# Kernel tuning notes

Measured on AMD Instinct MI355X. Metric: run time of the kernel, lower is better.

## Reference

```python
import jax, jax.numpy as jnp
import numpy as np

NB_OBJECTS = 3
DIM_BODY = 10
DIM_OBJECT = 15
DIM_OBJ_FEAT = NB_OBJECTS + DIM_OBJECT  # 18
DIM_PHI_IN = 54
HID = 256
DIM_PHI_OUT = 256
DIM_RHO_OUT = 1
B = 65536

# (o1, o2) object pair and (j, k) predicate indices, as in the torch code
PAIRS = [((0, 1), (3, 5)), ((0, 2), (4, 7)), ((1, 2), (6, 8))]


def setup_inputs() -> dict:
    key = jax.random.key(0)
    ks = jax.random.split(key, 24)
    inp = {
        "obs": jax.random.normal(ks[0], (B, 55), dtype=jnp.float32),
        "ag": jax.random.uniform(ks[1], (B, 9), dtype=jnp.float32),
        "g": jax.random.uniform(ks[2], (B, 9), dtype=jnp.float32),
        "anchor_g": jax.random.uniform(ks[3], (B, 9), dtype=jnp.float32),
        "act": jax.random.normal(ks[4], (B, 4), dtype=jnp.float32),
    }
    s = 0.05
    # PhiCriticDeepSet: two independent 2-layer MLPs (streams 1 and 2)
    inp["w1"] = jax.random.normal(ks[5], (DIM_PHI_IN, HID), dtype=jnp.float32) * s
    inp["b1"] = jnp.zeros((HID,), dtype=jnp.float32)
    inp["w2"] = jax.random.normal(ks[6], (HID, DIM_PHI_OUT), dtype=jnp.float32) * s
    inp["b2"] = jnp.zeros((DIM_PHI_OUT,), dtype=jnp.float32)
    inp["w3"] = jax.random.normal(ks[7], (DIM_PHI_IN, HID), dtype=jnp.float32) * s
    inp["b3"] = jnp.zeros((HID,), dtype=jnp.float32)
    inp["w4"] = jax.random.normal(ks[8], (HID, DIM_PHI_OUT), dtype=jnp.float32) * s
    inp["b4"] = jnp.zeros((DIM_PHI_OUT,), dtype=jnp.float32)
    # RhoCriticDeepSet: two independent 2-layer heads
    inp["w5"] = jax.random.normal(ks[9], (DIM_PHI_OUT, HID), dtype=jnp.float32) * s
    inp["b5"] = jnp.zeros((HID,), dtype=jnp.float32)
    inp["w6"] = jax.random.normal(ks[10], (HID, DIM_RHO_OUT), dtype=jnp.float32) * s
    inp["b6"] = jnp.zeros((DIM_RHO_OUT,), dtype=jnp.float32)
    inp["w7"] = jax.random.normal(ks[11], (DIM_PHI_OUT, HID), dtype=jnp.float32) * s
    inp["b7"] = jnp.zeros((HID,), dtype=jnp.float32)
    inp["w8"] = jax.random.normal(ks[12], (HID, DIM_RHO_OUT), dtype=jnp.float32) * s
    inp["b8"] = jnp.zeros((DIM_RHO_OUT,), dtype=jnp.float32)
    return inp


def _build_pair_inputs(obs, ag, g, act, anchor_g):
    """combinations_trick branch: data-dependent gather of goal bits and object pairs."""
    bs = obs.shape[0]
    obs_body = obs[:, :DIM_BODY]
    eye = jnp.eye(NB_OBJECTS, dtype=obs.dtype)
    # obs_objects: [3, B, 18] = one-hot(3) ++ object state(15)
    obs_objects = jnp.stack([
        jnp.concatenate([jnp.broadcast_to(eye[i], (bs, NB_OBJECTS)),
                         obs[:, DIM_BODY + DIM_OBJECT * i: DIM_BODY + DIM_OBJECT * (i + 1)]],
                        axis=1)
        for i in range(NB_OBJECTS)], axis=0)
    bidx = jnp.arange(bs)
    inputs = []
    for i, ((o1, o2), (j, k)) in enumerate(PAIRS):
        # selector = anchor_g @ [e_j, e_k] difference = anchor_g[:, j] - anchor_g[:, k]
        sel = (anchor_g[:, j] - anchor_g[:, k]) >= 0  # [B] bool
        # idxs_bits[i] = [i, j] where sel else [i, k]
        bit2 = jnp.where(sel, j, k)  # [B] int
        ag_pair = jnp.stack([ag[:, i], ag[bidx, bit2]], axis=1)  # [B, 2]
        g_pair = jnp.stack([g[:, i], g[bidx, bit2]], axis=1)     # [B, 2]
        # idxs_objects[i] = [o1, o2] where sel else [o2, o1]
        oi = jnp.where(sel, o1, o2)  # [B]
        oj = jnp.where(sel, o2, o1)
        obj_first = obs_objects[oi, bidx]   # [B, 18] gather along object axis
        obj_second = obs_objects[oj, bidx]  # [B, 18]
        inputs.append(jnp.concatenate(
            [ag_pair, g_pair, obs_body, obj_first, obj_second, act], axis=1))
    return jnp.stack(inputs)  # [3, B, 54]


def reference(obs, ag, g, anchor_g, act,
              w1, b1, w2, b2, w3, b3, w4, b4,
              w5, b5, w6, b6, w7, b7, w8, b8):
    inp = _build_pair_inputs(obs, ag, g, act, anchor_g)  # [3, B, 54]
    # PhiCriticDeepSet (two relu-relu streams)
    x1 = jax.nn.relu(jnp.einsum('pbi,ih->pbh', jax.nn.relu(jnp.einsum('pbd,dh->pbh', inp, w1) + b1), w2) + b2)
    x2 = jax.nn.relu(jnp.einsum('pbi,ih->pbh', jax.nn.relu(jnp.einsum('pbd,dh->pbh', inp, w3) + b3), w4) + b4)
    s1 = x1.sum(axis=0)  # [B, 256] deepset sum over pairs
    s2 = x2.sum(axis=0)
    # RhoCriticDeepSet readouts
    q1 = jax.nn.relu(s1 @ w5 + b5) @ w6 + b6  # [B, 1]
    q2 = jax.nn.relu(s2 @ w7 + b7) @ w8 + b8  # [B, 1]
    return (q1, q2)
```

## Files before the change

### kernel.cpp

```cpp
#include <hip/hip_runtime.h>

typedef unsigned short u16;
typedef unsigned int   u32;

using bf8 = __attribute__((ext_vector_type(8))) __bf16;
using f4  = __attribute__((ext_vector_type(4))) float;

__device__ __forceinline__ float b2f(u16 u) {
    union { u32 i; float f; } v; v.i = ((u32)u) << 16; return v.f;
}
__device__ __forceinline__ u16 f2b(float f) {
    union { float f; u32 i; } v; v.f = f;
    u32 x = v.i;
    x += 0x7fffu + ((x >> 16) & 1u);
    return (u16)(x >> 16);
}

__global__ void swz_all(const float* __restrict__ w1, const float* __restrict__ w3,
                        const float* __restrict__ w2, const float* __restrict__ w4,
                        const float* __restrict__ w5, const float* __restrict__ w7,
                        u16* __restrict__ ws) {
    int bid = blockIdx.x;
    const float* src; u16* dst; int kmax; int rel;
    if      (bid <  32) { src = w1; dst = ws;          kmax = 54;  rel = bid;       }
    else if (bid <  64) { src = w3; dst = ws + 16384;  kmax = 54;  rel = bid - 32;  }
    else if (bid < 192) { src = w2; dst = ws + 32768;  kmax = 256; rel = bid - 64;  }
    else if (bid < 320) { src = w4; dst = ws + 98304;  kmax = 256; rel = bid - 192; }
    else if (bid < 448) { src = w5; dst = ws + 163840; kmax = 256; rel = bid - 320; }
    else                { src = w7; dst = ws + 229376; kmax = 256; rel = bid - 448; }
    int kt = rel >> 4, ct = rel & 15, lane = threadIdx.x;
    int n = ct * 16 + (lane & 15);
    int kbase = kt * 32 + (lane >> 4) * 8;
    u16* d = dst + (size_t)(rel * 64 + lane) * 8;
    #pragma unroll
    for (int j = 0; j < 8; ++j) {
        int k = kbase + j;
        d[j] = (k < kmax) ? f2b(src[k * 256 + n]) : (u16)0;
    }
}

__global__ __launch_bounds__(256, 2) void critic_kernel(
    const float* __restrict__ obs, const float* __restrict__ ag,
    const float* __restrict__ g,   const float* __restrict__ anchor,
    const float* __restrict__ act,
    const float* __restrict__ b1,  const float* __restrict__ b2,
    const float* __restrict__ b3,  const float* __restrict__ b4,
    const float* __restrict__ b5,  const float* __restrict__ b7,
    const float* __restrict__ w6,  const float* __restrict__ b6,
    const float* __restrict__ w8,  const float* __restrict__ b8,
    const u16* __restrict__ wsz, float* __restrict__ out, int B) {

    __shared__ u16 inp_lds[96 * 72];
    __shared__ u16 h_lds[96 * 264];

    const int t    = threadIdx.x;
    const int lane = t & 63;
    const int wave = t >> 6;
    const int lr   = lane & 15;
    const int lg   = lane >> 4;
    const int wg   = blockIdx.x;

    if (t < 96) {
        const int O1[3] = {0, 0, 1}, O2[3] = {1, 2, 2};
        const int JA[3] = {3, 4, 6}, KA[3] = {5, 7, 8};
        int p = t / 32, bl = t % 32;
        int b = wg * 32 + bl;
        int j = JA[p], k = KA[p];
        bool sel = (anchor[b * 9 + j] - anchor[b * 9 + k]) >= 0.0f;
        int bit2 = sel ? j : k;
        int oi = sel ? O1[p] : O2[p];
        int oj = sel ? O2[p] : O1[p];
        u16* row = &inp_lds[t * 72];
        row[0] = f2b(ag[b * 9 + p]);
        row[1] = f2b(ag[b * 9 + bit2]);
        row[2] = f2b(g[b * 9 + p]);
        row[3] = f2b(g[b * 9 + bit2]);
        for (int c = 0; c < 10; ++c) row[4 + c] = f2b(obs[b * 55 + c]);
        const u16 ONE = 0x3F80;
        row[14] = (oi == 0) ? ONE : 0; row[15] = (oi == 1) ? ONE : 0; row[16] = (oi == 2) ? ONE : 0;
        for (int c = 0; c < 15; ++c) row[17 + c] = f2b(obs[b * 55 + 10 + 15 * oi + c]);
        row[32] = (oj == 0) ? ONE : 0; row[33] = (oj == 1) ? ONE : 0; row[34] = (oj == 2) ? ONE : 0;
        for (int c = 0; c < 15; ++c) row[35 + c] = f2b(obs[b * 55 + 10 + 15 * oj + c]);
        for (int c = 0; c < 4; ++c)  row[50 + c] = f2b(act[b * 4 + c]);
        for (int c = 54; c < 72; ++c) row[c] = 0;
    }
    __syncthreads();

    f4  sacc[2][4];
    u32 s1p[2][4][2];

    for (int net = 0; net < 2; ++net) {
        const u16* Wl1 = wsz + (net ? 16384 : 0);
        const u16* Wl2 = wsz + 32768 + (net ? 65536 : 0);
        const float* bl1 = net ? b3 : b1;
        const float* bl2 = net ? b4 : b2;

        f4 acc[6][4];
        #pragma unroll
        for (int rt = 0; rt < 6; ++rt)
            #pragma unroll
            for (int c = 0; c < 4; ++c) acc[rt][c] = (f4){0.f, 0.f, 0.f, 0.f};
        #pragma unroll
        for (int kt = 0; kt < 2; ++kt) {
            bf8 bfr[4];
            #pragma unroll
            for (int c = 0; c < 4; ++c)
                bfr[c] = *(const bf8*)(Wl1 + (size_t)(((kt * 16 + wave * 4 + c) * 64 + lane) * 8));
            #pragma unroll
            for (int rt = 0; rt < 6; ++rt) {
                bf8 afr = *(const bf8*)(&inp_lds[(rt * 16 + lr) * 72 + kt * 32 + lg * 8]);
                #pragma unroll
                for (int c = 0; c < 4; ++c)
                    acc[rt][c] = __builtin_amdgcn_mfma_f32_16x16x32_bf16(afr, bfr[c], acc[rt][c], 0, 0, 0);
            }
        }
        #pragma unroll
        for (int c = 0; c < 4; ++c) {
            float bias = bl1[(wave * 4 + c) * 16 + lr];
            #pragma unroll
            for (int rt = 0; rt < 6; ++rt)
                #pragma unroll
                for (int r = 0; r < 4; ++r) {
                    float x = acc[rt][c][r] + bias;
                    h_lds[(rt * 16 + lg * 4 + r) * 264 + (wave * 4 + c) * 16 + lr] = f2b(fmaxf(x, 0.f));
                }
        }
        __syncthreads();

        f4 acc2[6][4];
        #pragma unroll
        for (int rt = 0; rt < 6; ++rt)
            #pragma unroll
            for (int c = 0; c < 4; ++c) acc2[rt][c] = (f4){0.f, 0.f, 0.f, 0.f};
        #pragma unroll
        for (int ks = 0; ks < 8; ++ks) {
            bf8 bfr[4];
            #pragma unroll
            for (int c = 0; c < 4; ++c)
                bfr[c] = *(const bf8*)(Wl2 + (size_t)(((ks * 16 + wave * 4 + c) * 64 + lane) * 8));
            #pragma unroll
            for (int rt = 0; rt < 6; ++rt) {
                bf8 afr = *(const bf8*)(&h_lds[(rt * 16 + lr) * 264 + ks * 32 + lg * 8]);
                #pragma unroll
                for (int c = 0; c < 4; ++c)
                    acc2[rt][c] = __builtin_amdgcn_mfma_f32_16x16x32_bf16(afr, bfr[c], acc2[rt][c], 0, 0, 0);
            }
        }
        #pragma unroll
        for (int c = 0; c < 4; ++c) {
            float bias = bl2[(wave * 4 + c) * 16 + lr];
            #pragma unroll
            for (int s = 0; s < 2; ++s) {
                f4 sv = (f4){0.f, 0.f, 0.f, 0.f};
                #pragma unroll
                for (int p = 0; p < 3; ++p)
                    #pragma unroll
                    for (int r = 0; r < 4; ++r)
                        sv[r] += fmaxf(acc2[p * 2 + s][c][r] + bias, 0.f);
                if (net == 0) {
                    s1p[s][c][0] = (u32)f2b(sv[0]) | ((u32)f2b(sv[1]) << 16);
                    s1p[s][c][1] = (u32)f2b(sv[2]) | ((u32)f2b(sv[3]) << 16);
                } else {
                    sacc[s][c] = sv;
                }
            }
        }
        __syncthreads();
    }

    #pragma unroll
    for (int s = 0; s < 2; ++s)
        #pragma unroll
        for (int c = 0; c < 4; ++c) {
            int col = (wave * 4 + c) * 16 + lr;
            #pragma unroll
            for (int r = 0; r < 4; ++r) {
                int rowo = (s * 16 + lg * 4 + r) * 264 + col;
                h_lds[rowo]        = (u16)(s1p[s][c][r >> 1] >> ((r & 1) * 16));
                h_lds[8448 + rowo] = f2b(sacc[s][c][r]);
            }
        }
    __syncthreads();

    for (int net = 0; net < 2; ++net) {
        const u16* Wr = wsz + 163840 + net * 65536;
        const float* br = net ? b7 : b5;
        const int soff = net ? 8448 : 0;
        const int hoff = net ? 0 : 16896;
        f4 racc[2][4];
        #pragma unroll
        for (int rt = 0; rt < 2; ++rt)
            #pragma unroll
            for (int c = 0; c < 4; ++c) racc[rt][c] = (f4){0.f, 0.f, 0.f, 0.f};
        #pragma unroll
        for (int ks = 0; ks < 8; ++ks) {
            bf8 bfr[4];
            #pragma unroll
            for (int c = 0; c < 4; ++c)
                bfr[c] = *(const bf8*)(Wr + (size_t)(((ks * 16 + wave * 4 + c) * 64 + lane) * 8));
            #pragma unroll
            for (int rt = 0; rt < 2; ++rt) {
                bf8 afr = *(const bf8*)(&h_lds[soff + (rt * 16 + lr) * 264 + ks * 32 + lg * 8]);
                #pragma unroll
                for (int c = 0; c < 4; ++c)
                    racc[rt][c] = __builtin_amdgcn_mfma_f32_16x16x32_bf16(afr, bfr[c], racc[rt][c], 0, 0, 0);
            }
        }
        #pragma unroll
        for (int c = 0; c < 4; ++c) {
            float bias = br[(wave * 4 + c) * 16 + lr];
            #pragma unroll
            for (int rt = 0; rt < 2; ++rt)
                #pragma unroll
                for (int r = 0; r < 4; ++r) {
                    float x = fmaxf(racc[rt][c][r] + bias, 0.f);
                    h_lds[hoff + (rt * 16 + lg * 4 + r) * 264 + (wave * 4 + c) * 16 + lr] = f2b(x);
                }
        }
        __syncthreads();
    }

    if (t < 64) {
        int net = t >> 5, r = t & 31;
        const float* wv = net ? w8 : w6;
        const int hoff = net ? 0 : 16896;
        float q = net ? b8[0] : b6[0];
        #pragma unroll 8
        for (int kk = 0; kk < 256; ++kk)
            q += b2f(h_lds[hoff + r * 264 + kk]) * wv[kk];
        out[net * B + wg * 32 + r] = q;
    }
}

extern "C" void kernel_launch(void* const* d_in, const int* in_sizes, int n_in,
                              void* d_out, int out_size, void* d_ws, size_t ws_size,
                              hipStream_t stream) {
    const float* obs = (const float*)d_in[0];
    const float* ag  = (const float*)d_in[1];
    const float* g   = (const float*)d_in[2];
    const float* anc = (const float*)d_in[3];
    const float* act = (const float*)d_in[4];
    const float* w1  = (const float*)d_in[5];
    const float* b1  = (const float*)d_in[6];
    const float* w2  = (const float*)d_in[7];
    const float* b2  = (const float*)d_in[8];
    const float* w3  = (const float*)d_in[9];
    const float* b3  = (const float*)d_in[10];
    const float* w4  = (const float*)d_in[11];
    const float* b4  = (const float*)d_in[12];
    const float* w5  = (const float*)d_in[13];
    const float* b5  = (const float*)d_in[14];
    const float* w6  = (const float*)d_in[15];
    const float* b6  = (const float*)d_in[16];
    const float* w7  = (const float*)d_in[17];
    const float* b7  = (const float*)d_in[18];
    const float* w8  = (const float*)d_in[19];
    const float* b8  = (const float*)d_in[20];
    u16* ws   = (u16*)d_ws;
    float* out = (float*)d_out;
    int B = in_sizes[0] / 55;

    swz_all<<<576, 64, 0, stream>>>(w1, w3, w2, w4, w5, w7, ws);
    critic_kernel<<<(B + 31) / 32, 256, 0, stream>>>(obs, ag, g, anc, act,
                                                     b1, b2, b3, b4, b5, b7,
                                                     w6, b6, w8, b8, ws, out, B);
}
```

Before: 219.1 us.

## Coalesce input staging, fuse rho heads, parallelize final dot, retile weight swizzle

Inputs for each 32-row block are now loaded with coalesced strided loops into a shared staging area, and pair rows are built from LDS instead of scattered global reads. The two rho readout GEMMs are merged into one loop so both weight sets are loaded together, which removes a barrier pass. The final 256-wide dot products are split across all four waves and reduced through LDS rather than computed serially by 64 threads. The weight swizzle kernel now uses float4 coalesced loads through a shared slab with fewer, larger blocks. The cost is more shared-memory traffic and extra barriers at the start of the kernel.

```diff
diff --git a/kernel.cpp b/kernel.cpp
--- a/kernel.cpp
+++ b/kernel.cpp
@@ -1,4 +1,5 @@
 #include <hip/hip_runtime.h>
+#include <hip/hip_bf16.h>
 
 typedef unsigned short u16;
 typedef unsigned int   u32;
@@ -15,29 +16,59 @@
     x += 0x7fffu + ((x >> 16) & 1u);
     return (u16)(x >> 16);
 }
+__device__ __forceinline__ u32 pk2(float lo, float hi) {
+    union { __hip_bfloat162 h; u32 u; } v;
+    v.h = __float22bfloat162_rn(make_float2(lo, hi));
+    return v.u;
+}
 
 __global__ void swz_all(const float* __restrict__ w1, const float* __restrict__ w3,
                         const float* __restrict__ w2, const float* __restrict__ w4,
                         const float* __restrict__ w5, const float* __restrict__ w7,
                         u16* __restrict__ ws) {
-    int bid = blockIdx.x;
-    const float* src; u16* dst; int kmax; int rel;
-    if      (bid <  32) { src = w1; dst = ws;          kmax = 54;  rel = bid;       }
-    else if (bid <  64) { src = w3; dst = ws + 16384;  kmax = 54;  rel = bid - 32;  }
-    else if (bid < 192) { src = w2; dst = ws + 32768;  kmax = 256; rel = bid - 64;  }
-    else if (bid < 320) { src = w4; dst = ws + 98304;  kmax = 256; rel = bid - 192; }
-    else if (bid < 448) { src = w5; dst = ws + 163840; kmax = 256; rel = bid - 320; }
-    else                { src = w7; dst = ws + 229376; kmax = 256; rel = bid - 448; }
-    int kt = rel >> 4, ct = rel & 15, lane = threadIdx.x;
-    int n = ct * 16 + (lane & 15);
-    int kbase = kt * 32 + (lane >> 4) * 8;
-    u16* d = dst + (size_t)(rel * 64 + lane) * 8;
+    __shared__ u16 slab[32 * 270];
+    int b = blockIdx.x, t = threadIdx.x;
+    const float* src; u16* dst; int kmax, kt;
+    if      (b <  2) { src = w1; dst = ws;          kmax = 54;  kt = b;      }
+    else if (b <  4) { src = w3; dst = ws + 16384;  kmax = 54;  kt = b - 2;  }
+    else if (b < 12) { src = w2; dst = ws + 32768;  kmax = 256; kt = b - 4;  }
+    else if (b < 20) { src = w4; dst = ws + 98304;  kmax = 256; kt = b - 12; }
+    else if (b < 28) { src = w5; dst = ws + 163840; kmax = 256; kt = b - 20; }
+    else             { src = w7; dst = ws + 229376; kmax = 256; kt = b - 28; }
+
     #pragma unroll
-    for (int j = 0; j < 8; ++j) {
-        int k = kbase + j;
-        d[j] = (k < kmax) ? f2b(src[k * 256 + n]) : (u16)0;
-    }
-}
+    for (int it = 0; it < 8; ++it) {
+        int flat = it * 1024 + t * 4;
+        int row = flat >> 8, col = flat & 255;
+        int k = kt * 32 + row;
+        float4 v = make_float4(0.f, 0.f, 0.f, 0.f);
+        if (k < kmax) v = *(const float4*)(src + k * 256 + col);
+        u32* sp = (u32*)&slab[row * 270 + col];
+        sp[0] = pk2(v.x, v.y);
+        sp[1] = pk2(v.z, v.w);
+    }
+    __syncthreads();
+
+    int lane = t & 63, wave = t >> 6, lr = lane & 15, kg = lane >> 4;
+    #pragma unroll
+    for (int i = 0; i < 4; ++i) {
+        int ct = wave * 4 + i;
+        u16 v[8];
+        #pragma unroll
+        for (int j = 0; j < 8; ++j)
+            v[j] = slab[(kg * 8 + j) * 270 + ct * 16 + lr];
+        uint4 o;
+        o.x = (u32)v[0] | ((u32)v[1] << 16);
+        o.y = (u32)v[2] | ((u32)v[3] << 16);
+        o.z = (u32)v[4] | ((u32)v[5] << 16);
+        o.w = (u32)v[6] | ((u32)v[7] << 16);
+        *(uint4*)(dst + (size_t)(((kt * 16 + ct) * 64 + lane) * 8)) = o;
+    }
+}
+
+#define H_OFF 6912
+#define RH0   (H_OFF + 16896)
+#define RH1   (H_OFF + 16)
 
 __global__ __launch_bounds__(256, 2) void critic_kernel(
     const float* __restrict__ obs, const float* __restrict__ ag,
@@ -50,8 +81,7 @@
     const float* __restrict__ w8,  const float* __restrict__ b8,
     const u16* __restrict__ wsz, float* __restrict__ out, int B) {
 
-    __shared__ u16 inp_lds[96 * 72];
-    __shared__ u16 h_lds[96 * 264];
+    __shared__ u16 pool[32256];
 
     const int t    = threadIdx.x;
     const int lane = t & 63;
@@ -60,29 +90,51 @@
     const int lg   = lane >> 4;
     const int wg   = blockIdx.x;
 
+    const int STG = H_OFF;
+    for (int i = t; i < 1760; i += 256) {
+        int b = i / 55, c = i - b * 55;
+        pool[STG + b * 56 + c] = f2b(obs[wg * 1760 + i]);
+    }
+    for (int i = t; i < 288; i += 256) {
+        int b = i / 9, c = i - b * 9;
+        pool[STG + 1792 + b * 10 + c] = f2b(ag[wg * 288 + i]);
+    }
+    for (int i = t; i < 288; i += 256) {
+        int b = i / 9, c = i - b * 9;
+        pool[STG + 2112 + b * 10 + c] = f2b(g[wg * 288 + i]);
+    }
+    if (t < 128)
+        pool[STG + 2432 + t] = f2b(act[wg * 128 + t]);
+    for (int i = t; i < 288; i += 256) {
+        int b = i / 9, c = i - b * 9;
+        ((u32*)pool)[(STG + 2560) / 2 + b * 10 + c] = __float_as_uint(anchor[wg * 288 + i]);
+    }
+    __syncthreads();
+
     if (t < 96) {
         const int O1[3] = {0, 0, 1}, O2[3] = {1, 2, 2};
         const int JA[3] = {3, 4, 6}, KA[3] = {5, 7, 8};
         int p = t / 32, bl = t % 32;
-        int b = wg * 32 + bl;
         int j = JA[p], k = KA[p];
-        bool sel = (anchor[b * 9 + j] - anchor[b * 9 + k]) >= 0.0f;
+        float aj = __uint_as_float(((u32*)pool)[(STG + 2560) / 2 + bl * 10 + j]);
+        float ak = __uint_as_float(((u32*)pool)[(STG + 2560) / 2 + bl * 10 + k]);
+        bool sel = (aj - ak) >= 0.0f;
         int bit2 = sel ? j : k;
         int oi = sel ? O1[p] : O2[p];
         int oj = sel ? O2[p] : O1[p];
-        u16* row = &inp_lds[t * 72];
-        row[0] = f2b(ag[b * 9 + p]);
-        row[1] = f2b(ag[b * 9 + bit2]);
-        row[2] = f2b(g[b * 9 + p]);
-        row[3] = f2b(g[b * 9 + bit2]);
-        for (int c = 0; c < 10; ++c) row[4 + c] = f2b(obs[b * 55 + c]);
+        u16* row = &pool[t * 72];
+        row[0] = pool[STG + 1792 + bl * 10 + p];
+        row[1] = pool[STG + 1792 + bl * 10 + bit2];
+        row[2] = pool[STG + 2112 + bl * 10 + p];
+        row[3] = pool[STG + 2112 + bl * 10 + bit2];
+        for (int c = 0; c < 10; ++c) row[4 + c] = pool[STG + bl * 56 + c];
         const u16 ONE = 0x3F80;
         row[14] = (oi == 0) ? ONE : 0; row[15] = (oi == 1) ? ONE : 0; row[16] = (oi == 2) ? ONE : 0;
-        for (int c = 0; c < 15; ++c) row[17 + c] = f2b(obs[b * 55 + 10 + 15 * oi + c]);
+        for (int c = 0; c < 15; ++c) row[17 + c] = pool[STG + bl * 56 + 10 + 15 * oi + c];
         row[32] = (oj == 0) ? ONE : 0; row[33] = (oj == 1) ? ONE : 0; row[34] = (oj == 2) ? ONE : 0;
-        for (int c = 0; c < 15; ++c) row[35 + c] = f2b(obs[b * 55 + 10 + 15 * oj + c]);
-        for (int c = 0; c < 4; ++c)  row[50 + c] = f2b(act[b * 4 + c]);
-        for (int c = 54; c < 72; ++c) row[c] = 0;
+        for (int c = 0; c < 15; ++c) row[35 + c] = pool[STG + bl * 56 + 10 + 15 * oj + c];
+        for (int c = 0; c < 4; ++c)  row[50 + c] = pool[STG + 2432 + bl * 4 + c];
+        for (int c = 54; c < 64; ++c) row[c] = 0;
     }
     __syncthreads();
 
@@ -108,7 +160,7 @@
                 bfr[c] = *(const bf8*)(Wl1 + (size_t)(((kt * 16 + wave * 4 + c) * 64 + lane) * 8));
             #pragma unroll
             for (int rt = 0; rt < 6; ++rt) {
-                bf8 afr = *(const bf8*)(&inp_lds[(rt * 16 + lr) * 72 + kt * 32 + lg * 8]);
+                bf8 afr = *(const bf8*)(&pool[(rt * 16 + lr) * 72 + kt * 32 + lg * 8]);
                 #pragma unroll
                 for (int c = 0; c < 4; ++c)
                     acc[rt][c] = __builtin_amdgcn_mfma_f32_16x16x32_bf16(afr, bfr[c], acc[rt][c], 0, 0, 0);
@@ -118,12 +170,15 @@
         for (int c = 0; c < 4; ++c) {
             float bias = bl1[(wave * 4 + c) * 16 + lr];
             #pragma unroll
-            for (int rt = 0; rt < 6; ++rt)
-                #pragma unroll
-                for (int r = 0; r < 4; ++r) {
-                    float x = acc[rt][c][r] + bias;
-                    h_lds[(rt * 16 + lg * 4 + r) * 264 + (wave * 4 + c) * 16 + lr] = f2b(fmaxf(x, 0.f));
-                }
+            for (int rt = 0; rt < 6; ++rt) {
+                u32 p01 = pk2(fmaxf(acc[rt][c][0] + bias, 0.f), fmaxf(acc[rt][c][1] + bias, 0.f));
+                u32 p23 = pk2(fmaxf(acc[rt][c][2] + bias, 0.f), fmaxf(acc[rt][c][3] + bias, 0.f));
+                int base = H_OFF + (rt * 16 + lg * 4) * 264 + (wave * 4 + c) * 16 + lr;
+                pool[base]           = (u16)p01;
+                pool[base + 264]     = (u16)(p01 >> 16);
+                pool[base + 2 * 264] = (u16)p23;
+                pool[base + 3 * 264] = (u16)(p23 >> 16);
+            }
         }
         __syncthreads();
 
@@ -140,7 +195,7 @@
                 bfr[c] = *(const bf8*)(Wl2 + (size_t)(((ks * 16 + wave * 4 + c) * 64 + lane) * 8));
             #pragma unroll
             for (int rt = 0; rt < 6; ++rt) {
-                bf8 afr = *(const bf8*)(&h_lds[(rt * 16 + lr) * 264 + ks * 32 + lg * 8]);
+                bf8 afr = *(const bf8*)(&pool[H_OFF + (rt * 16 + lr) * 264 + ks * 32 + lg * 8]);
                 #pragma unroll
                 for (int c = 0; c < 4; ++c)
                     acc2[rt][c] = __builtin_amdgcn_mfma_f32_16x16x32_bf16(afr, bfr[c], acc2[rt][c], 0, 0, 0);
@@ -158,8 +213,8 @@
                     for (int r = 0; r < 4; ++r)
                         sv[r] += fmaxf(acc2[p * 2 + s][c][r] + bias, 0.f);
                 if (net == 0) {
-                    s1p[s][c][0] = (u32)f2b(sv[0]) | ((u32)f2b(sv[1]) << 16);
-                    s1p[s][c][1] = (u32)f2b(sv[2]) | ((u32)f2b(sv[3]) << 16);
+                    s1p[s][c][0] = pk2(sv[0], sv[1]);
+                    s1p[s][c][1] = pk2(sv[2], sv[3]);
                 } else {
                     sacc[s][c] = sv;
                 }
@@ -173,62 +228,107 @@
         #pragma unroll
         for (int c = 0; c < 4; ++c) {
             int col = (wave * 4 + c) * 16 + lr;
-            #pragma unroll
-            for (int r = 0; r < 4; ++r) {
-                int rowo = (s * 16 + lg * 4 + r) * 264 + col;
-                h_lds[rowo]        = (u16)(s1p[s][c][r >> 1] >> ((r & 1) * 16));
-                h_lds[8448 + rowo] = f2b(sacc[s][c][r]);
-            }
-        }
-    __syncthreads();
-
-    for (int net = 0; net < 2; ++net) {
-        const u16* Wr = wsz + 163840 + net * 65536;
-        const float* br = net ? b7 : b5;
-        const int soff = net ? 8448 : 0;
-        const int hoff = net ? 0 : 16896;
-        f4 racc[2][4];
-        #pragma unroll
-        for (int rt = 0; rt < 2; ++rt)
+            u32 a01 = pk2(sacc[s][c][0], sacc[s][c][1]);
+            u32 a23 = pk2(sacc[s][c][2], sacc[s][c][3]);
+            int base = H_OFF + (s * 16 + lg * 4) * 264 + col;
+            pool[base]                  = (u16)s1p[s][c][0];
+            pool[base + 264]            = (u16)(s1p[s][c][0] >> 16);
+            pool[base + 2 * 264]        = (u16)s1p[s][c][1];
+            pool[base + 3 * 264]        = (u16)(s1p[s][c][1] >> 16);
+            pool[base + 8448]           = (u16)a01;
+            pool[base + 8448 + 264]     = (u16)(a01 >> 16);
+            pool[base + 8448 + 2 * 264] = (u16)a23;
+            pool[base + 8448 + 3 * 264] = (u16)(a23 >> 16);
+        }
+    __syncthreads();
+
+    {
+        const u16* W5 = wsz + 163840;
+        const u16* W7 = wsz + 229376;
+        f4 racc[4][4];
+        #pragma unroll
+        for (int rt = 0; rt < 4; ++rt)
             #pragma unroll
             for (int c = 0; c < 4; ++c) racc[rt][c] = (f4){0.f, 0.f, 0.f, 0.f};
         #pragma unroll
         for (int ks = 0; ks < 8; ++ks) {
-            bf8 bfr[4];
-            #pragma unroll
-            for (int c = 0; c < 4; ++c)
-                bfr[c] = *(const bf8*)(Wr + (size_t)(((ks * 16 + wave * 4 + c) * 64 + lane) * 8));
+            bf8 bfr5[4], bfr7[4];
+            #pragma unroll
+            for (int c = 0; c < 4; ++c) {
+                size_t off = (size_t)(((ks * 16 + wave * 4 + c) * 64 + lane) * 8);
+                bfr5[c] = *(const bf8*)(W5 + off);
+                bfr7[c] = *(const bf8*)(W7 + off);
+            }
             #pragma unroll
             for (int rt = 0; rt < 2; ++rt) {
-                bf8 afr = *(const bf8*)(&h_lds[soff + (rt * 16 + lr) * 264 + ks * 32 + lg * 8]);
+                bf8 a1 = *(const bf8*)(&pool[H_OFF + (rt * 16 + lr) * 264 + ks * 32 + lg * 8]);
+                bf8 a2 = *(const bf8*)(&pool[H_OFF + 8448 + (rt * 16 + lr) * 264 + ks * 32 + lg * 8]);
                 #pragma unroll
-                for (int c = 0; c < 4; ++c)
-                    racc[rt][c] = __builtin_amdgcn_mfma_f32_16x16x32_bf16(afr, bfr[c], racc[rt][c], 0, 0, 0);
-            }
-        }
-        #pragma unroll
-        for (int c = 0; c < 4; ++c) {
-            float bias = br[(wave * 4 + c) * 16 + lr];
-            #pragma unroll
-            for (int rt = 0; rt < 2; ++rt)
-                #pragma unroll
-                for (int r = 0; r < 4; ++r) {
-                    float x = fmaxf(racc[rt][c][r] + bias, 0.f);
-                    h_lds[hoff + (rt * 16 + lg * 4 + r) * 264 + (wave * 4 + c) * 16 + lr] = f2b(x);
+                for (int c = 0; c < 4; ++c) {
+                    racc[rt][c]     = __builtin_amdgcn_mfma_f32_16x16x32_bf16(a1, bfr5[c], racc[rt][c], 0, 0, 0);
+                    racc[2 + rt][c] = __builtin_amdgcn_mfma_f32_16x16x32_bf16(a2, bfr7[c], racc[2 + rt][c], 0, 0, 0);
                 }
-        }
-        __syncthreads();
-    }
-
+            }
+        }
+        #pragma unroll
+        for (int c = 0; c < 4; ++c) {
+            float bias = b5[(wave * 4 + c) * 16 + lr];
+            #pragma unroll
+            for (int rt = 0; rt < 2; ++rt) {
+                u32 p01 = pk2(fmaxf(racc[rt][c][0] + bias, 0.f), fmaxf(racc[rt][c][1] + bias, 0.f));
+                u32 p23 = pk2(fmaxf(racc[rt][c][2] + bias, 0.f), fmaxf(racc[rt][c][3] + bias, 0.f));
+                int base = RH0 + (rt * 16 + lg * 4) * 264 + (wave * 4 + c) * 16 + lr;
+                pool[base]           = (u16)p01;
+                pool[base + 264]     = (u16)(p01 >> 16);
+                pool[base + 2 * 264] = (u16)p23;
+                pool[base + 3 * 264] = (u16)(p23 >> 16);
+            }
+        }
+        __syncthreads();
+        #pragma unroll
+        for (int c = 0; c < 4; ++c) {
+            float bias = b7[(wave * 4 + c) * 16 + lr];
+            #pragma unroll
+            for (int rt = 0; rt < 2; ++rt) {
+                u32 p01 = pk2(fmaxf(racc[2 + rt][c][0] + bias, 0.f), fmaxf(racc[2 + rt][c][1] + bias, 0.f));
+                u32 p23 = pk2(fmaxf(racc[2 + rt][c][2] + bias, 0.f), fmaxf(racc[2 + rt][c][3] + bias, 0.f));
+                int base = RH1 + (rt * 16 + lg * 4) * 264 + (wave * 4 + c) * 16 + lr;
+                pool[base]           = (u16)p01;
+                pool[base + 264]     = (u16)(p01 >> 16);
+                pool[base + 2 * 264] = (u16)p23;
+                pool[base + 3 * 264] = (u16)(p23 >> 16);
+            }
+        }
+        __syncthreads();
+    }
+
+    {
+        int q = wave;
+        int net = lane >> 5, r = lane & 31;
+        int hoff = net ? RH1 : RH0;
+        const float* wv = net ? w8 : w6;
+        float s = 0.f;
+        int base = hoff + r * 264 + q * 64;
+        #pragma unroll
+        for (int it = 0; it < 16; ++it) {
+            uint2 two = *(const uint2*)&pool[base + it * 4];
+            float4 wq = *(const float4*)(wv + q * 64 + it * 4);
+            s += __uint_as_float(two.x << 16)          * wq.x;
+            s += __uint_as_float(two.x & 0xffff0000u)  * wq.y;
+            s += __uint_as_float(two.y << 16)          * wq.z;
+            s += __uint_as_float(two.y & 0xffff0000u)  * wq.w;
+        }
+        __syncthreads();
+        ((u32*)pool)[t] = __float_as_uint(s);
+    }
+    __syncthreads();
     if (t < 64) {
         int net = t >> 5, r = t & 31;
-        const float* wv = net ? w8 : w6;
-        const int hoff = net ? 0 : 16896;
-        float q = net ? b8[0] : b6[0];
-        #pragma unroll 8
-        for (int kk = 0; kk < 256; ++kk)
-            q += b2f(h_lds[hoff + r * 264 + kk]) * wv[kk];
-        out[net * B + wg * 32 + r] = q;
+        float qv = net ? b8[0] : b6[0];
+        #pragma unroll
+        for (int p = 0; p < 4; ++p)
+            qv += __uint_as_float(((u32*)pool)[p * 64 + net * 32 + r]);
+        out[net * B + wg * 32 + r] = qv;
     }
 }
 
@@ -256,11 +356,11 @@
     const float* b7  = (const float*)d_in[18];
     const float* w8  = (const float*)d_in[19];
     const float* b8  = (const float*)d_in[20];
-    u16* ws   = (u16*)d_ws;
+    u16* ws    = (u16*)d_ws;
     float* out = (float*)d_out;
     int B = in_sizes[0] / 55;
 
-    swz_all<<<576, 64, 0, stream>>>(w1, w3, w2, w4, w5, w7, ws);
+    swz_all<<<36, 256, 0, stream>>>(w1, w3, w2, w4, w5, w7, ws);
     critic_kernel<<<(B + 31) / 32, 256, 0, stream>>>(obs, ag, g, anc, act,
                                                      b1, b2, b3, b4, b5, b7,
                                                      w6, b6, w8, b8, ws, out, B);
```

Result: no change. 223.3 us (+1.9%).
